# Kernel tuning notes

Measured on AMD Instinct MI355X. Metric: run time of the kernel, lower is better.

Reference implementation:

```python
import jax, jax.numpy as jnp
import numpy as np

B, S, D_MODEL, D_QK, D_VO = 4, 2048, 1024, 128, 128
NEG = -1.0e9


def setup_inputs() -> dict:
    key = jax.random.key(0)
    k1, k2, k3, k4, k5 = jax.random.split(key, 5)
    enc = jax.random.normal(k1, (B, S, D_MODEL), dtype=jnp.float32)
    # causal mask: True means masked (masked_fill), broadcast over batch
    causal = jnp.triu(jnp.ones((S, S), dtype=bool), k=1)
    mask = jnp.broadcast_to(causal, (B, S, S))
    scale = 0.02
    W_q = jax.random.normal(k2, (D_MODEL, D_QK), dtype=jnp.float32) * scale
    W_k = jax.random.normal(k3, (D_MODEL, D_QK), dtype=jnp.float32) * scale
    W_v = jax.random.normal(k4, (D_MODEL, D_VO), dtype=jnp.float32) * scale
    W_o = jax.random.normal(k5, (D_VO, D_MODEL), dtype=jnp.float32) * scale
    return {"encodings": enc, "mask": mask, "W_q": W_q, "W_k": W_k, "W_v": W_v, "W_o": W_o}


def reference(encodings, mask, W_q, W_k, W_v, W_o):
    # q,k: [B,S,d_qk]; v: [B,S,d_vo]
    q = jnp.einsum('bsd,de->bse', encodings, W_q)
    k = jnp.einsum('bsd,de->bse', encodings, W_k)
    v = jnp.einsum('bsd,de->bse', encodings, W_v)
    sims = jnp.einsum('bqe,bke->bqk', q, k) / jnp.asarray(D_QK ** 0.5, q.dtype)
    sims = jnp.where(mask, jnp.asarray(NEG, sims.dtype), sims)
    attn = jax.nn.softmax(sims, axis=-1)  # [B,S,S]
    scores = jnp.einsum('bqk,bke->bqe', attn, v)  # [B,S,d_vo]
    return jnp.einsum('bse,ed->bsd', scores, W_o)  # [B,S,d_model]
```

## Files before the change

kernel.cpp:

```cpp
#include <hip/hip_runtime.h>
#include <hip/hip_bf16.h>
#include <stdint.h>

typedef __attribute__((ext_vector_type(8))) short short8;
typedef __attribute__((ext_vector_type(4))) float floatx4;

using bf16 = __hip_bfloat16;

#define SCALE_L2 0.12751793359133147f

__device__ inline unsigned short f2b(float f) {
    bf16 h = __float2bfloat16(f);
    return *(unsigned short*)&h;
}
__device__ inline float b2f(unsigned short u) {
    union { unsigned int i; float f; } v;
    v.i = ((unsigned int)u) << 16;
    return v.f;
}

__global__ __launch_bounds__(256) void prep_w(const float* __restrict__ Wq,
                                              const float* __restrict__ Wk,
                                              const float* __restrict__ Wv,
                                              const float* __restrict__ Wo,
                                              bf16* __restrict__ Wqkvt,
                                              bf16* __restrict__ Wot) {
    int idx4 = (blockIdx.x * 256 + threadIdx.x) * 4;
    int sel = idx4 >> 17;
    int i = idx4 & 131071;
    if (sel < 3) {
        const float* W = (sel == 0) ? Wq : (sel == 1) ? Wk : Wv;
        float4 v = *(const float4*)&W[i];
        int r = i >> 7, c = i & 127;
        Wqkvt[(size_t)(sel * 128 + c + 0) * 1024 + r] = __float2bfloat16(v.x);
        Wqkvt[(size_t)(sel * 128 + c + 1) * 1024 + r] = __float2bfloat16(v.y);
        Wqkvt[(size_t)(sel * 128 + c + 2) * 1024 + r] = __float2bfloat16(v.z);
        Wqkvt[(size_t)(sel * 128 + c + 3) * 1024 + r] = __float2bfloat16(v.w);
    } else {
        float4 v = *(const float4*)&Wo[i];
        int r = i >> 10, c = i & 1023;
        Wot[(size_t)(c + 0) * 128 + r] = __float2bfloat16(v.x);
        Wot[(size_t)(c + 1) * 128 + r] = __float2bfloat16(v.y);
        Wot[(size_t)(c + 2) * 128 + r] = __float2bfloat16(v.z);
        Wot[(size_t)(c + 3) * 128 + r] = __float2bfloat16(v.w);
    }
}

__global__ __launch_bounds__(256) void gemm_qkv(const float* __restrict__ enc,
                                                const bf16* __restrict__ Bt,
                                                bf16* __restrict__ Qb,
                                                bf16* __restrict__ Kb,
                                                bf16* __restrict__ Vtb) {
    __shared__ bf16 As[64 * 40];
    __shared__ bf16 Bs[64 * 40];

    const int tid = threadIdx.x;
    const int m0 = blockIdx.x * 64;
    const int brow0 = blockIdx.y * 64;
    const int proj = brow0 >> 7;
    const int colb = brow0 & 127;
    const int w = tid >> 6, lane = tid & 63;
    const int wm = (w >> 1) * 32, wn = (w & 1) * 32;
    const int quad = lane >> 4, l16 = lane & 15;

    const int ra = tid >> 2, kq = (tid & 3) * 8;

    floatx4 acc[2][2];
#pragma unroll
    for (int i = 0; i < 2; i++)
#pragma unroll
        for (int j = 0; j < 2; j++) acc[i][j] = (floatx4){0.f, 0.f, 0.f, 0.f};

    float4 pa0 = *(const float4*)&enc[(size_t)(m0 + ra) * 1024 + kq];
    float4 pa1 = *(const float4*)&enc[(size_t)(m0 + ra) * 1024 + kq + 4];
    int4 pb = *(const int4*)&Bt[(size_t)(brow0 + ra) * 1024 + kq];

    for (int k0 = 0; k0 < 1024; k0 += 32) {
        __syncthreads();
        short8 av;
        av[0] = (short)f2b(pa0.x); av[1] = (short)f2b(pa0.y);
        av[2] = (short)f2b(pa0.z); av[3] = (short)f2b(pa0.w);
        av[4] = (short)f2b(pa1.x); av[5] = (short)f2b(pa1.y);
        av[6] = (short)f2b(pa1.z); av[7] = (short)f2b(pa1.w);
        *(short8*)&As[ra * 40 + kq] = av;
        *(int4*)&Bs[ra * 40 + kq] = pb;
        __syncthreads();

        if (k0 + 32 < 1024) {
            pa0 = *(const float4*)&enc[(size_t)(m0 + ra) * 1024 + k0 + 32 + kq];
            pa1 = *(const float4*)&enc[(size_t)(m0 + ra) * 1024 + k0 + 36 + kq];
            pb = *(const int4*)&Bt[(size_t)(brow0 + ra) * 1024 + k0 + 32 + kq];
        }

        short8 a[2], b[2];
#pragma unroll
        for (int mt = 0; mt < 2; mt++)
            a[mt] = *(const short8*)&As[(wm + mt * 16 + l16) * 40 + quad * 8];
#pragma unroll
        for (int nt = 0; nt < 2; nt++)
            b[nt] = *(const short8*)&Bs[(wn + nt * 16 + l16) * 40 + quad * 8];
#pragma unroll
        for (int mt = 0; mt < 2; mt++)
#pragma unroll
            for (int nt = 0; nt < 2; nt++)
                acc[mt][nt] = __builtin_amdgcn_mfma_f32_16x16x32_bf16(a[mt], b[nt], acc[mt][nt], 0, 0, 0);
    }

#pragma unroll
    for (int mt = 0; mt < 2; mt++)
#pragma unroll
        for (int nt = 0; nt < 2; nt++)
#pragma unroll
            for (int r = 0; r < 4; r++) {
                int row = m0 + wm + mt * 16 + quad * 4 + r;
                int col = colb + wn + nt * 16 + l16;
                bf16 h = __float2bfloat16(acc[mt][nt][r]);
                if (proj == 0) {
                    Qb[(size_t)row * 128 + col] = h;
                } else if (proj == 1) {
                    Kb[(size_t)row * 128 + col] = h;
                } else {
                    int bb = row >> 11, ss = row & 2047;
                    Vtb[(size_t)bb * 262144 + (size_t)col * 2048 + ss] = h;
                }
            }
}

__global__ __launch_bounds__(256) void flash_split(const bf16* __restrict__ Q,
                                                   const bf16* __restrict__ K,
                                                   const bf16* __restrict__ Vt,
                                                   bf16* __restrict__ Opb,
                                                   float2* __restrict__ Ml) {
    __shared__ bf16 Ks[64 * 136];
    __shared__ bf16 Vs[128 * 72];
    __shared__ bf16 Ps[4 * 16 * 72];

    const int tid = threadIdx.x;
    const int x = blockIdx.x;
    const int b = x / 272;
    const int id = x - b * 272;
    int m = (int)((__builtin_sqrtf(4.0f * (float)id + 1.0f) - 1.0f) * 0.5f);
    while ((m + 1) * (m + 2) <= id) m++;
    while (m * (m + 1) > id) m--;
    const int rem = id - m * (m + 1);
    const int qt = (rem < m + 1) ? 2 * m : 2 * m + 1;
    const int c = (rem < m + 1) ? rem : rem - (m + 1);
    const int q0 = qt * 64;
    const int start = 2 * c;
    const int end = min(start + 2, qt + 1);

    const int w = tid >> 6, lane = tid & 63;
    const int quad = lane >> 4, l16 = lane & 15;

    const int qrow = q0 + w * 16 + l16;
    const bf16* Qrow = &Q[((size_t)b * 2048 + qrow) * 128];
    short8 qf[4];
#pragma unroll
    for (int k4 = 0; k4 < 4; k4++)
        qf[k4] = *(const short8*)&Qrow[k4 * 32 + quad * 8];

    float m_run = -1.0e30f, l_run = 0.f;
    floatx4 o[8];
#pragma unroll
    for (int d = 0; d < 8; d++) o[d] = (floatx4){0.f, 0.f, 0.f, 0.f};

    int4 kreg[4], vreg[4];
    const int sr[4]  = {(tid + 0) >> 4, (tid + 256) >> 4, (tid + 512) >> 4, (tid + 768) >> 4};
    const int scg    = (tid & 15) * 8;
    const int sr2[4] = {(tid + 0) >> 3, (tid + 256) >> 3, (tid + 512) >> 3, (tid + 768) >> 3};
    const int scg2   = (tid & 7) * 8;

#pragma unroll
    for (int i = 0; i < 4; i++) {
        kreg[i] = *(const int4*)&K[((size_t)b * 2048 + start * 64 + sr[i]) * 128 + scg];
        vreg[i] = *(const int4*)&Vt[(size_t)b * 262144 + (size_t)sr2[i] * 2048 + start * 64 + scg2];
    }

    for (int kt = start; kt < end; kt++) {
        __syncthreads();
#pragma unroll
        for (int i = 0; i < 4; i++) {
            *(int4*)&Ks[sr[i] * 136 + scg] = kreg[i];
            *(int4*)&Vs[sr2[i] * 72 + scg2] = vreg[i];
        }
        __syncthreads();

        if (kt + 1 < end) {
#pragma unroll
            for (int i = 0; i < 4; i++) {
                kreg[i] = *(const int4*)&K[((size_t)b * 2048 + (kt + 1) * 64 + sr[i]) * 128 + scg];
                vreg[i] = *(const int4*)&Vt[(size_t)b * 262144 + (size_t)sr2[i] * 2048 + (kt + 1) * 64 + scg2];
            }
        }

        floatx4 s_acc[4];
#pragma unroll
        for (int nt = 0; nt < 4; nt++) {
            s_acc[nt] = (floatx4){0.f, 0.f, 0.f, 0.f};
#pragma unroll
            for (int k4 = 0; k4 < 4; k4++) {
                short8 kf = *(const short8*)&Ks[(nt * 16 + l16) * 136 + k4 * 32 + quad * 8];
                s_acc[nt] = __builtin_amdgcn_mfma_f32_16x16x32_bf16(kf, qf[k4], s_acc[nt], 0, 0, 0);
            }
        }

        float sv[4][4];
#pragma unroll
        for (int nt = 0; nt < 4; nt++)
#pragma unroll
            for (int r = 0; r < 4; r++) {
                float s = s_acc[nt][r] * SCALE_L2;
                if (kt == qt) {
                    int kcol = kt * 64 + nt * 16 + quad * 4 + r;
                    if (kcol > qrow) s = -1.0e9f;
                }
                sv[nt][r] = s;
            }

        float t0 = fmaxf(fmaxf(sv[0][0], sv[0][1]), fmaxf(sv[0][2], sv[0][3]));
        float t1 = fmaxf(fmaxf(sv[1][0], sv[1][1]), fmaxf(sv[1][2], sv[1][3]));
        float t2 = fmaxf(fmaxf(sv[2][0], sv[2][1]), fmaxf(sv[2][2], sv[2][3]));
        float t3 = fmaxf(fmaxf(sv[3][0], sv[3][1]), fmaxf(sv[3][2], sv[3][3]));
        float tmax = fmaxf(fmaxf(t0, t1), fmaxf(t2, t3));
        tmax = fmaxf(tmax, __shfl_xor(tmax, 16));
        tmax = fmaxf(tmax, __shfl_xor(tmax, 32));

        float mnew = fmaxf(m_run, tmax);
        float alpha = exp2f(m_run - mnew);
        m_run = mnew;

        float rsum = 0.f;
#pragma unroll
        for (int nt = 0; nt < 4; nt++)
#pragma unroll
            for (int r = 0; r < 4; r++) {
                float p = exp2f(sv[nt][r] - mnew);
                sv[nt][r] = p;
                rsum += p;
            }
        rsum += __shfl_xor(rsum, 16);
        rsum += __shfl_xor(rsum, 32);
        l_run = l_run * alpha + rsum;

#pragma unroll
        for (int nt = 0; nt < 4; nt++) {
            ushort4 pk;
            pk.x = f2b(sv[nt][0]); pk.y = f2b(sv[nt][1]);
            pk.z = f2b(sv[nt][2]); pk.w = f2b(sv[nt][3]);
            *(ushort4*)&Ps[w * 1152 + l16 * 72 + nt * 16 + quad * 4] = pk;
        }

#pragma unroll
        for (int d = 0; d < 8; d++) {
            o[d][0] *= alpha; o[d][1] *= alpha; o[d][2] *= alpha; o[d][3] *= alpha;
        }

        short8 pf[2];
#pragma unroll
        for (int k2 = 0; k2 < 2; k2++)
            pf[k2] = *(const short8*)&Ps[w * 1152 + l16 * 72 + k2 * 32 + quad * 8];
#pragma unroll
        for (int d = 0; d < 8; d++)
#pragma unroll
            for (int k2 = 0; k2 < 2; k2++) {
                short8 vf = *(const short8*)&Vs[(d * 16 + l16) * 72 + k2 * 32 + quad * 8];
                o[d] = __builtin_amdgcn_mfma_f32_16x16x32_bf16(vf, pf[k2], o[d], 0, 0, 0);
            }
    }

    const int lrow = w * 16 + l16;
    const size_t obase = ((size_t)x * 64 + lrow) * 128;
#pragma unroll
    for (int d = 0; d < 8; d++) {
        ushort4 pk;
        pk.x = f2b(o[d][0]); pk.y = f2b(o[d][1]);
        pk.z = f2b(o[d][2]); pk.w = f2b(o[d][3]);
        *(ushort4*)&Opb[obase + d * 16 + quad * 4] = pk;
    }
    if (lane < 16) Ml[(size_t)x * 64 + lrow] = make_float2(m_run, l_run);
}

__global__ __launch_bounds__(256) void gemm_out_merge(const bf16* __restrict__ Opb,
                                                      const float2* __restrict__ Ml,
                                                      const bf16* __restrict__ Bt,
                                                      float* __restrict__ C) {
    __shared__ bf16 As[64 * 40];
    __shared__ bf16 Bs[128 * 40];

    const int tid = threadIdx.x;
    const int m0 = blockIdx.x * 64;
    const int n0 = blockIdx.y * 128;
    const int w = tid >> 6, lane = tid & 63;
    const int wm = (w >> 1) * 32, wn = (w & 1) * 64;
    const int quad = lane >> 4, l16 = lane & 15;

    const int ra = tid >> 2, kq = (tid & 3) * 8;
    const int rb0 = tid >> 2, rb1 = (tid + 256) >> 2;

    const int row = m0 + ra;
    const int bb = row >> 11, s = row & 2047;
    const int qt = s >> 6, rl = s & 63;
    const int mm = qt >> 1;
    const int nc = mm + 1;
    const int id0 = bb * 272 + mm * (mm + 1) + ((qt & 1) ? (mm + 1) : 0);

    float M = -1.0e30f;
    for (int j = 0; j < nc; j++)
        M = fmaxf(M, Ml[(size_t)(id0 + j) * 64 + rl].x);
    float wgt[16];
    float L = 0.f;
    for (int j = 0; j < nc; j++) {
        float2 t = Ml[(size_t)(id0 + j) * 64 + rl];
        float wj = exp2f(t.x - M);
        wgt[j] = wj;
        L += t.y * wj;
    }
    float inv = 1.0f / L;
    for (int j = 0; j < nc; j++) wgt[j] *= inv;

    floatx4 acc[2][4];
#pragma unroll
    for (int i = 0; i < 2; i++)
#pragma unroll
        for (int j = 0; j < 4; j++) acc[i][j] = (floatx4){0.f, 0.f, 0.f, 0.f};

    int4 pb0 = *(const int4*)&Bt[(size_t)(n0 + rb0) * 128 + kq];
    int4 pb1 = *(const int4*)&Bt[(size_t)(n0 + rb1) * 128 + kq];

    for (int k0 = 0; k0 < 128; k0 += 32) {
        float a8[8] = {0.f, 0.f, 0.f, 0.f, 0.f, 0.f, 0.f, 0.f};
        const int dq = k0 + kq;
        for (int j = 0; j < nc; j++) {
            const ushort4* p = (const ushort4*)&Opb[((size_t)(id0 + j) * 64 + rl) * 128 + dq];
            ushort4 p0 = p[0], p1 = p[1];
            float wj = wgt[j];
            a8[0] += wj * b2f(p0.x); a8[1] += wj * b2f(p0.y);
            a8[2] += wj * b2f(p0.z); a8[3] += wj * b2f(p0.w);
            a8[4] += wj * b2f(p1.x); a8[5] += wj * b2f(p1.y);
            a8[6] += wj * b2f(p1.z); a8[7] += wj * b2f(p1.w);
        }
        short8 av;
#pragma unroll
        for (int e = 0; e < 8; e++) av[e] = (short)f2b(a8[e]);

        __syncthreads();
        *(short8*)&As[ra * 40 + kq] = av;
        *(int4*)&Bs[rb0 * 40 + kq] = pb0;
        *(int4*)&Bs[rb1 * 40 + kq] = pb1;
        __syncthreads();

        if (k0 + 32 < 128) {
            pb0 = *(const int4*)&Bt[(size_t)(n0 + rb0) * 128 + k0 + 32 + kq];
            pb1 = *(const int4*)&Bt[(size_t)(n0 + rb1) * 128 + k0 + 32 + kq];
        }

        short8 a[2], b[4];
#pragma unroll
        for (int mt = 0; mt < 2; mt++)
            a[mt] = *(const short8*)&As[(wm + mt * 16 + l16) * 40 + quad * 8];
#pragma unroll
        for (int nt = 0; nt < 4; nt++)
            b[nt] = *(const short8*)&Bs[(wn + nt * 16 + l16) * 40 + quad * 8];
#pragma unroll
        for (int mt = 0; mt < 2; mt++)
#pragma unroll
            for (int nt = 0; nt < 4; nt++)
                acc[mt][nt] = __builtin_amdgcn_mfma_f32_16x16x32_bf16(a[mt], b[nt], acc[mt][nt], 0, 0, 0);
    }

#pragma unroll
    for (int mt = 0; mt < 2; mt++)
#pragma unroll
        for (int nt = 0; nt < 4; nt++)
#pragma unroll
            for (int r = 0; r < 4; r++) {
                int orow = m0 + wm + mt * 16 + quad * 4 + r;
                int ocol = n0 + wn + nt * 16 + l16;
                C[(size_t)orow * 1024 + ocol] = acc[mt][nt][r];
            }
}

extern "C" void kernel_launch(void* const* d_in, const int* in_sizes, int n_in,
                              void* d_out, int out_size, void* d_ws, size_t ws_size,
                              hipStream_t stream) {
    const float* enc = (const float*)d_in[0];
    const float* Wq = (const float*)d_in[2];
    const float* Wk = (const float*)d_in[3];
    const float* Wv = (const float*)d_in[4];
    const float* Wo = (const float*)d_in[5];
    float* out = (float*)d_out;

    const size_t MB = 1024 * 1024;
    char* ws = (char*)d_ws;
    bf16*   Opb   = (bf16*)(ws);
    bf16*   Qb    = (bf16*)(ws + 18 * MB);
    bf16*   Kb    = (bf16*)(ws + 20 * MB);
    bf16*   Vtb   = (bf16*)(ws + 22 * MB);
    bf16*   Wqkvt = (bf16*)(ws + 24 * MB);
    bf16*   Wot   = (bf16*)(ws + 24 * MB + 768 * 1024);
    float2* Ml    = (float2*)(ws + 25 * MB);

    dim3 blk(256);
    prep_w<<<512, blk, 0, stream>>>(Wq, Wk, Wv, Wo, Wqkvt, Wot);

    gemm_qkv<<<dim3(128, 6), blk, 0, stream>>>(enc, Wqkvt, Qb, Kb, Vtb);

    flash_split<<<1088, blk, 0, stream>>>(Qb, Kb, Vtb, Opb, Ml);

    gemm_out_merge<<<dim3(128, 8), blk, 0, stream>>>(Opb, Ml, Wot, out);
}
```

Baseline: 219.4 us.

## Fuse all stages into one persistent kernel with grid-wide atomic barriers

Replaces the four separate launches (weight prep, QKV GEMM, split flash attention, merge+output GEMM) with a single persistent kernel of 512 blocks that loops over tiles and uses atomic-counter grid barriers between stages. The flash split changes from chunks of two key tiles to chunks of three, and the merge now appears to be a separate stage writing a bf16 scores buffer before a plain output GEMM. The aim is to remove launch gaps and tail effects between kernels. In exchange it adds spin-wait barrier overhead and a memset, it relies on all 512 blocks being co-resident, and it gives less parallelism per stage.

```diff
diff --git a/kernel.cpp b/kernel.cpp
--- a/kernel.cpp
+++ b/kernel.cpp
@@ -8,6 +8,8 @@
 using bf16 = __hip_bfloat16;
 
 #define SCALE_L2 0.12751793359133147f
+
+#define GRID 512
 
 __device__ inline unsigned short f2b(float f) {
     bf16 h = __float2bfloat16(f);
@@ -19,365 +21,383 @@
     return v.f;
 }
 
-__global__ __launch_bounds__(256) void prep_w(const float* __restrict__ Wq,
-                                              const float* __restrict__ Wk,
-                                              const float* __restrict__ Wv,
-                                              const float* __restrict__ Wo,
-                                              bf16* __restrict__ Wqkvt,
-                                              bf16* __restrict__ Wot) {
-    int idx4 = (blockIdx.x * 256 + threadIdx.x) * 4;
-    int sel = idx4 >> 17;
-    int i = idx4 & 131071;
-    if (sel < 3) {
-        const float* W = (sel == 0) ? Wq : (sel == 1) ? Wk : Wv;
-        float4 v = *(const float4*)&W[i];
-        int r = i >> 7, c = i & 127;
-        Wqkvt[(size_t)(sel * 128 + c + 0) * 1024 + r] = __float2bfloat16(v.x);
-        Wqkvt[(size_t)(sel * 128 + c + 1) * 1024 + r] = __float2bfloat16(v.y);
-        Wqkvt[(size_t)(sel * 128 + c + 2) * 1024 + r] = __float2bfloat16(v.z);
-        Wqkvt[(size_t)(sel * 128 + c + 3) * 1024 + r] = __float2bfloat16(v.w);
-    } else {
-        float4 v = *(const float4*)&Wo[i];
-        int r = i >> 10, c = i & 1023;
-        Wot[(size_t)(c + 0) * 128 + r] = __float2bfloat16(v.x);
-        Wot[(size_t)(c + 1) * 128 + r] = __float2bfloat16(v.y);
-        Wot[(size_t)(c + 2) * 128 + r] = __float2bfloat16(v.z);
-        Wot[(size_t)(c + 3) * 128 + r] = __float2bfloat16(v.w);
-    }
-}
-
-__global__ __launch_bounds__(256) void gemm_qkv(const float* __restrict__ enc,
-                                                const bf16* __restrict__ Bt,
-                                                bf16* __restrict__ Qb,
-                                                bf16* __restrict__ Kb,
-                                                bf16* __restrict__ Vtb) {
-    __shared__ bf16 As[64 * 40];
-    __shared__ bf16 Bs[64 * 40];
-
+__device__ inline int cum3(int qt) {
+    int a = qt / 3, r = qt - 3 * a;
+    return 3 * a * (a + 1) / 2 + r * (a + 1);
+}
+
+__device__ __forceinline__ void gbar(unsigned* bar, unsigned target) {
+    __threadfence();
+    __syncthreads();
+    if (threadIdx.x == 0) {
+        __hip_atomic_fetch_add(bar, 1u, __ATOMIC_RELEASE, __HIP_MEMORY_SCOPE_AGENT);
+        while (__hip_atomic_load(bar, __ATOMIC_ACQUIRE, __HIP_MEMORY_SCOPE_AGENT) < target)
+            __builtin_amdgcn_s_sleep(2);
+    }
+    __syncthreads();
+    __threadfence();
+}
+
+__global__ __launch_bounds__(256, 3) void mega(const float* __restrict__ enc,
+                                               const float* __restrict__ Wq,
+                                               const float* __restrict__ Wk,
+                                               const float* __restrict__ Wv,
+                                               const float* __restrict__ Wo,
+                                               bf16* __restrict__ Wqkvt,
+                                               bf16* __restrict__ Wot,
+                                               bf16* __restrict__ Qb,
+                                               bf16* __restrict__ Kb,
+                                               bf16* __restrict__ Vtb,
+                                               bf16* __restrict__ Opb,
+                                               float2* __restrict__ Ml,
+                                               bf16* __restrict__ Scb,
+                                               float* __restrict__ out,
+                                               unsigned* __restrict__ bar) {
+    __shared__ __align__(16) bf16 smem[22528];
+
+    const int bid = blockIdx.x;
     const int tid = threadIdx.x;
-    const int m0 = blockIdx.x * 64;
-    const int brow0 = blockIdx.y * 64;
-    const int proj = brow0 >> 7;
-    const int colb = brow0 & 127;
-    const int w = tid >> 6, lane = tid & 63;
-    const int wm = (w >> 1) * 32, wn = (w & 1) * 32;
-    const int quad = lane >> 4, l16 = lane & 15;
-
-    const int ra = tid >> 2, kq = (tid & 3) * 8;
-
-    floatx4 acc[2][2];
-#pragma unroll
-    for (int i = 0; i < 2; i++)
-#pragma unroll
-        for (int j = 0; j < 2; j++) acc[i][j] = (floatx4){0.f, 0.f, 0.f, 0.f};
-
-    float4 pa0 = *(const float4*)&enc[(size_t)(m0 + ra) * 1024 + kq];
-    float4 pa1 = *(const float4*)&enc[(size_t)(m0 + ra) * 1024 + kq + 4];
-    int4 pb = *(const int4*)&Bt[(size_t)(brow0 + ra) * 1024 + kq];
-
-    for (int k0 = 0; k0 < 1024; k0 += 32) {
-        __syncthreads();
-        short8 av;
-        av[0] = (short)f2b(pa0.x); av[1] = (short)f2b(pa0.y);
-        av[2] = (short)f2b(pa0.z); av[3] = (short)f2b(pa0.w);
-        av[4] = (short)f2b(pa1.x); av[5] = (short)f2b(pa1.y);
-        av[6] = (short)f2b(pa1.z); av[7] = (short)f2b(pa1.w);
-        *(short8*)&As[ra * 40 + kq] = av;
-        *(int4*)&Bs[ra * 40 + kq] = pb;
-        __syncthreads();
-
-        if (k0 + 32 < 1024) {
-            pa0 = *(const float4*)&enc[(size_t)(m0 + ra) * 1024 + k0 + 32 + kq];
-            pa1 = *(const float4*)&enc[(size_t)(m0 + ra) * 1024 + k0 + 36 + kq];
-            pb = *(const int4*)&Bt[(size_t)(brow0 + ra) * 1024 + k0 + 32 + kq];
-        }
-
-        short8 a[2], b[2];
-#pragma unroll
-        for (int mt = 0; mt < 2; mt++)
-            a[mt] = *(const short8*)&As[(wm + mt * 16 + l16) * 40 + quad * 8];
-#pragma unroll
-        for (int nt = 0; nt < 2; nt++)
-            b[nt] = *(const short8*)&Bs[(wn + nt * 16 + l16) * 40 + quad * 8];
-#pragma unroll
-        for (int mt = 0; mt < 2; mt++)
-#pragma unroll
-            for (int nt = 0; nt < 2; nt++)
-                acc[mt][nt] = __builtin_amdgcn_mfma_f32_16x16x32_bf16(a[mt], b[nt], acc[mt][nt], 0, 0, 0);
-    }
-
-#pragma unroll
-    for (int mt = 0; mt < 2; mt++)
-#pragma unroll
-        for (int nt = 0; nt < 2; nt++)
-#pragma unroll
-            for (int r = 0; r < 4; r++) {
-                int row = m0 + wm + mt * 16 + quad * 4 + r;
-                int col = colb + wn + nt * 16 + l16;
-                bf16 h = __float2bfloat16(acc[mt][nt][r]);
-                if (proj == 0) {
-                    Qb[(size_t)row * 128 + col] = h;
-                } else if (proj == 1) {
-                    Kb[(size_t)row * 128 + col] = h;
-                } else {
-                    int bb = row >> 11, ss = row & 2047;
-                    Vtb[(size_t)bb * 262144 + (size_t)col * 2048 + ss] = h;
-                }
-            }
-}
-
-__global__ __launch_bounds__(256) void flash_split(const bf16* __restrict__ Q,
-                                                   const bf16* __restrict__ K,
-                                                   const bf16* __restrict__ Vt,
-                                                   bf16* __restrict__ Opb,
-                                                   float2* __restrict__ Ml) {
-    __shared__ bf16 Ks[64 * 136];
-    __shared__ bf16 Vs[128 * 72];
-    __shared__ bf16 Ps[4 * 16 * 72];
-
-    const int tid = threadIdx.x;
-    const int x = blockIdx.x;
-    const int b = x / 272;
-    const int id = x - b * 272;
-    int m = (int)((__builtin_sqrtf(4.0f * (float)id + 1.0f) - 1.0f) * 0.5f);
-    while ((m + 1) * (m + 2) <= id) m++;
-    while (m * (m + 1) > id) m--;
-    const int rem = id - m * (m + 1);
-    const int qt = (rem < m + 1) ? 2 * m : 2 * m + 1;
-    const int c = (rem < m + 1) ? rem : rem - (m + 1);
-    const int q0 = qt * 64;
-    const int start = 2 * c;
-    const int end = min(start + 2, qt + 1);
-
     const int w = tid >> 6, lane = tid & 63;
     const int quad = lane >> 4, l16 = lane & 15;
 
-    const int qrow = q0 + w * 16 + l16;
-    const bf16* Qrow = &Q[((size_t)b * 2048 + qrow) * 128];
-    short8 qf[4];
-#pragma unroll
-    for (int k4 = 0; k4 < 4; k4++)
-        qf[k4] = *(const short8*)&Qrow[k4 * 32 + quad * 8];
-
-    float m_run = -1.0e30f, l_run = 0.f;
-    floatx4 o[8];
-#pragma unroll
-    for (int d = 0; d < 8; d++) o[d] = (floatx4){0.f, 0.f, 0.f, 0.f};
-
-    int4 kreg[4], vreg[4];
-    const int sr[4]  = {(tid + 0) >> 4, (tid + 256) >> 4, (tid + 512) >> 4, (tid + 768) >> 4};
-    const int scg    = (tid & 15) * 8;
-    const int sr2[4] = {(tid + 0) >> 3, (tid + 256) >> 3, (tid + 512) >> 3, (tid + 768) >> 3};
-    const int scg2   = (tid & 7) * 8;
-
-#pragma unroll
-    for (int i = 0; i < 4; i++) {
-        kreg[i] = *(const int4*)&K[((size_t)b * 2048 + start * 64 + sr[i]) * 128 + scg];
-        vreg[i] = *(const int4*)&Vt[(size_t)b * 262144 + (size_t)sr2[i] * 2048 + start * 64 + scg2];
-    }
-
-    for (int kt = start; kt < end; kt++) {
-        __syncthreads();
-#pragma unroll
-        for (int i = 0; i < 4; i++) {
-            *(int4*)&Ks[sr[i] * 136 + scg] = kreg[i];
-            *(int4*)&Vs[sr2[i] * 72 + scg2] = vreg[i];
+    {
+        int idx4 = (bid * 256 + tid) * 4;
+        int sel = idx4 >> 17;
+        int i = idx4 & 131071;
+        if (sel < 3) {
+            const float* W = (sel == 0) ? Wq : (sel == 1) ? Wk : Wv;
+            float4 v = *(const float4*)&W[i];
+            int r = i >> 7, c = i & 127;
+            Wqkvt[(size_t)(sel * 128 + c + 0) * 1024 + r] = __float2bfloat16(v.x);
+            Wqkvt[(size_t)(sel * 128 + c + 1) * 1024 + r] = __float2bfloat16(v.y);
+            Wqkvt[(size_t)(sel * 128 + c + 2) * 1024 + r] = __float2bfloat16(v.z);
+            Wqkvt[(size_t)(sel * 128 + c + 3) * 1024 + r] = __float2bfloat16(v.w);
+        } else {
+            float4 v = *(const float4*)&Wo[i];
+            int r = i >> 10, c = i & 1023;
+            Wot[(size_t)(c + 0) * 128 + r] = __float2bfloat16(v.x);
+            Wot[(size_t)(c + 1) * 128 + r] = __float2bfloat16(v.y);
+            Wot[(size_t)(c + 2) * 128 + r] = __float2bfloat16(v.z);
+            Wot[(size_t)(c + 3) * 128 + r] = __float2bfloat16(v.w);
         }
-        __syncthreads();
-
-        if (kt + 1 < end) {
+    }
+    gbar(bar, 1 * GRID);
+
+    {
+        bf16* As = smem;
+        bf16* Bs = smem + 2560;
+        const int wm = (w >> 1) * 32, wn = (w & 1) * 32;
+        const int ra = tid >> 2, kq = (tid & 3) * 8;
+
+        for (int t = bid; t < 768; t += GRID) {
+            const int m0 = (t & 127) * 64;
+            const int brow0 = (t >> 7) * 64;
+            const int proj = brow0 >> 7;
+            const int colb = brow0 & 127;
+
+            floatx4 acc[2][2];
+#pragma unroll
+            for (int i = 0; i < 2; i++)
+#pragma unroll
+                for (int j = 0; j < 2; j++) acc[i][j] = (floatx4){0.f, 0.f, 0.f, 0.f};
+
+            float4 pa0 = *(const float4*)&enc[(size_t)(m0 + ra) * 1024 + kq];
+            float4 pa1 = *(const float4*)&enc[(size_t)(m0 + ra) * 1024 + kq + 4];
+            int4 pb = *(const int4*)&Wqkvt[(size_t)(brow0 + ra) * 1024 + kq];
+
+            for (int k0 = 0; k0 < 1024; k0 += 32) {
+                __syncthreads();
+                short8 av;
+                av[0] = (short)f2b(pa0.x); av[1] = (short)f2b(pa0.y);
+                av[2] = (short)f2b(pa0.z); av[3] = (short)f2b(pa0.w);
+                av[4] = (short)f2b(pa1.x); av[5] = (short)f2b(pa1.y);
+                av[6] = (short)f2b(pa1.z); av[7] = (short)f2b(pa1.w);
+                *(short8*)&As[ra * 40 + kq] = av;
+                *(int4*)&Bs[ra * 40 + kq] = pb;
+                __syncthreads();
+
+                if (k0 + 32 < 1024) {
+                    pa0 = *(const float4*)&enc[(size_t)(m0 + ra) * 1024 + k0 + 32 + kq];
+                    pa1 = *(const float4*)&enc[(size_t)(m0 + ra) * 1024 + k0 + 36 + kq];
+                    pb = *(const int4*)&Wqkvt[(size_t)(brow0 + ra) * 1024 + k0 + 32 + kq];
+                }
+
+                short8 a[2], b[2];
+#pragma unroll
+                for (int mt = 0; mt < 2; mt++)
+                    a[mt] = *(const short8*)&As[(wm + mt * 16 + l16) * 40 + quad * 8];
+#pragma unroll
+                for (int nt = 0; nt < 2; nt++)
+                    b[nt] = *(const short8*)&Bs[(wn + nt * 16 + l16) * 40 + quad * 8];
+#pragma unroll
+                for (int mt = 0; mt < 2; mt++)
+#pragma unroll
+                    for (int nt = 0; nt < 2; nt++)
+                        acc[mt][nt] = __builtin_amdgcn_mfma_f32_16x16x32_bf16(a[mt], b[nt], acc[mt][nt], 0, 0, 0);
+            }
+
+#pragma unroll
+            for (int mt = 0; mt < 2; mt++)
+#pragma unroll
+                for (int nt = 0; nt < 2; nt++)
+#pragma unroll
+                    for (int r = 0; r < 4; r++) {
+                        int row = m0 + wm + mt * 16 + quad * 4 + r;
+                        int col = colb + wn + nt * 16 + l16;
+                        bf16 h = __float2bfloat16(acc[mt][nt][r]);
+                        if (proj == 0) {
+                            Qb[(size_t)row * 128 + col] = h;
+                        } else if (proj == 1) {
+                            Kb[(size_t)row * 128 + col] = h;
+                        } else {
+                            int bb = row >> 11, ss = row & 2047;
+                            Vtb[(size_t)bb * 262144 + (size_t)col * 2048 + ss] = h;
+                        }
+                    }
+            __syncthreads();
+        }
+    }
+    gbar(bar, 2 * GRID);
+
+    {
+        bf16* Ks = smem;
+        bf16* Vs = smem + 8704;
+        bf16* Ps = smem + 17920;
+        const int sr[4]  = {(tid + 0) >> 4, (tid + 256) >> 4, (tid + 512) >> 4, (tid + 768) >> 4};
+        const int scg    = (tid & 15) * 8;
+        const int sr2[4] = {(tid + 0) >> 3, (tid + 256) >> 3, (tid + 512) >> 3, (tid + 768) >> 3};
+        const int scg2   = (tid & 7) * 8;
+
+        for (int x = bid; x < 748; x += GRID) {
+            const int b = x / 187;
+            const int id = x - b * 187;
+            int qt = (int)__builtin_sqrtf(6.0f * (float)id + 1.0f);
+            if (qt > 31) qt = 31;
+            while (cum3(qt + 1) <= id) qt++;
+            while (cum3(qt) > id) qt--;
+            const int c = id - cum3(qt);
+            const int q0 = qt * 64;
+            const int start = 3 * c;
+            const int end = min(start + 3, qt + 1);
+
+            const int qrow = q0 + w * 16 + l16;
+            const bf16* Qrow = &Qb[((size_t)b * 2048 + qrow) * 128];
+            short8 qf[4];
+#pragma unroll
+            for (int k4 = 0; k4 < 4; k4++)
+                qf[k4] = *(const short8*)&Qrow[k4 * 32 + quad * 8];
+
+            float m_run = -1.0e30f, l_run = 0.f;
+            floatx4 o[8];
+#pragma unroll
+            for (int d = 0; d < 8; d++) o[d] = (floatx4){0.f, 0.f, 0.f, 0.f};
+
+            int4 kreg[4], vreg[4];
 #pragma unroll
             for (int i = 0; i < 4; i++) {
-                kreg[i] = *(const int4*)&K[((size_t)b * 2048 + (kt + 1) * 64 + sr[i]) * 128 + scg];
-                vreg[i] = *(const int4*)&Vt[(size_t)b * 262144 + (size_t)sr2[i] * 2048 + (kt + 1) * 64 + scg2];
-            }
+                kreg[i] = *(const int4*)&Kb[((size_t)b * 2048 + start * 64 + sr[i]) * 128 + scg];
+                vreg[i] = *(const int4*)&Vtb[(size_t)b * 262144 + (size_t)sr2[i] * 2048 + start * 64 + scg2];
+            }
+
+            for (int kt = start; kt < end; kt++) {
+                __syncthreads();
+#pragma unroll
+                for (int i = 0; i < 4; i++) {
+                    *(int4*)&Ks[sr[i] * 136 + scg] = kreg[i];
+                    *(int4*)&Vs[sr2[i] * 72 + scg2] = vreg[i];
+                }
+                __syncthreads();
+
+                if (kt + 1 < end) {
+#pragma unroll
+                    for (int i = 0; i < 4; i++) {
+                        kreg[i] = *(const int4*)&Kb[((size_t)b * 2048 + (kt + 1) * 64 + sr[i]) * 128 + scg];
+                        vreg[i] = *(const int4*)&Vtb[(size_t)b * 262144 + (size_t)sr2[i] * 2048 + (kt + 1) * 64 + scg2];
+                    }
+                }
+
+                floatx4 s_acc[4];
+#pragma unroll
+                for (int nt = 0; nt < 4; nt++) {
+                    s_acc[nt] = (floatx4){0.f, 0.f, 0.f, 0.f};
+#pragma unroll
+                    for (int k4 = 0; k4 < 4; k4++) {
+                        short8 kf = *(const short8*)&Ks[(nt * 16 + l16) * 136 + k4 * 32 + quad * 8];
+                        s_acc[nt] = __builtin_amdgcn_mfma_f32_16x16x32_bf16(kf, qf[k4], s_acc[nt], 0, 0, 0);
+                    }
+                }
+
+                float sv[4][4];
+#pragma unroll
+                for (int nt = 0; nt < 4; nt++)
+#pragma unroll
+                    for (int r = 0; r < 4; r++) {
+                        float s = s_acc[nt][r] * SCALE_L2;
+                        if (kt == qt) {
+                            int kcol = kt * 64 + nt * 16 + quad * 4 + r;
+                            if (kcol > qrow) s = -1.0e9f;
+                        }
+                        sv[nt][r] = s;
+                    }
+
+                float t0 = fmaxf(fmaxf(sv[0][0], sv[0][1]), fmaxf(sv[0][2], sv[0][3]));
+                float t1 = fmaxf(fmaxf(sv[1][0], sv[1][1]), fmaxf(sv[1][2], sv[1][3]));
+                float t2 = fmaxf(fmaxf(sv[2][0], sv[2][1]), fmaxf(sv[2][2], sv[2][3]));
+                float t3 = fmaxf(fmaxf(sv[3][0], sv[3][1]), fmaxf(sv[3][2], sv[3][3]));
+                float tmax = fmaxf(fmaxf(t0, t1), fmaxf(t2, t3));
+                tmax = fmaxf(tmax, __shfl_xor(tmax, 16));
+                tmax = fmaxf(tmax, __shfl_xor(tmax, 32));
+
+                float mnew = fmaxf(m_run, tmax);
+                float alpha = exp2f(m_run - mnew);
+                m_run = mnew;
+
+                float rsum = 0.f;
+#pragma unroll
+                for (int nt = 0; nt < 4; nt++)
+#pragma unroll
+                    for (int r = 0; r < 4; r++) {
+                        float p = exp2f(sv[nt][r] - mnew);
+                        sv[nt][r] = p;
+                        rsum += p;
+                    }
+                rsum += __shfl_xor(rsum, 16);
+                rsum += __shfl_xor(rsum, 32);
+                l_run = l_run * alpha + rsum;
+
+#pragma unroll
+                for (int nt = 0; nt < 4; nt++) {
+                    ushort4 pk;
+                    pk.x = f2b(sv[nt][0]); pk.y = f2b(sv[nt][1]);
+                    pk.z = f2b(sv[nt][2]); pk.w = f2b(sv[nt][3]);
+                    *(ushort4*)&Ps[w * 1152 + l16 * 72 + nt * 16 + quad * 4] = pk;
+                }
+
+#pragma unroll
+                for (int d = 0; d < 8; d++) {
+                    o[d][0] *= alpha; o[d][1] *= alpha; o[d][2] *= alpha; o[d][3] *= alpha;
+                }
+
+                short8 pf[2];
+#pragma unroll
+                for (int k2 = 0; k2 < 2; k2++)
+                    pf[k2] = *(const short8*)&Ps[w * 1152 + l16 * 72 + k2 * 32 + quad * 8];
+#pragma unroll
+                for (int d = 0; d < 8; d++)
+#pragma unroll
+                    for (int k2 = 0; k2 < 2; k2++) {
+                        short8 vf = *(const short8*)&Vs[(d * 16 + l16) * 72 + k2 * 32 + quad * 8];
+                        o[d] = __builtin_amdgcn_mfma_f32_16x16x32_bf16(vf, pf[k2], o[d], 0, 0, 0);
+                    }
+            }
+
+            const int lrow = w * 16 + l16;
+            const size_t obase = ((size_t)x * 64 + lrow) * 128;
+#pragma unroll
+            for (int d = 0; d < 8; d++) {
+                ushort4 pk;
+                pk.x = f2b(o[d][0]); pk.y = f2b(o[d][1]);
+                pk.z = f2b(o[d][2]); pk.w = f2b(o[d][3]);
+                *(ushort4*)&Opb[obase + d * 16 + quad * 4] = pk;
+            }
+            if (lane < 16) Ml[(size_t)x * 64 + lrow] = make_float2(m_run, l_run);
+            __syncthreads();
         }
-
-        floatx4 s_acc[4];
-#pragma unroll
-        for (int nt = 0; nt < 4; nt++) {
-            s_acc[nt] = (floatx4){0.f, 0.f, 0.f, 0.f};
-#pragma unroll
-            for (int k4 = 0; k4 < 4; k4++) {
-                short8 kf = *(const short8*)&Ks[(nt * 16 + l16) * 136 + k4 * 32 + quad * 8];
-                s_acc[nt] = __builtin_amdgcn_mfma_f32_16x16x32_bf16(kf, qf[k4], s_acc[nt], 0, 0, 0);
-            }
+    }
+    gbar(bar, 3 * GRID);
+
+    {
+        const int gtid = bid * 256 + tid;
+        for (int task = gtid; task < 262144; task += GRID * 256) {
+            int row = task >> 5, dg = (task & 31) * 4;
+            int b = row >> 11, s = row & 2047;
+            int qt = s >> 6, rl = s & 63;
+            int nc = (qt + 3) / 3;
+            int id0 = b * 187 + cum3(qt);
+
+            float M = -1.0e30f;
+            for (int j = 0; j < nc; j++)
+                M = fmaxf(M, Ml[(size_t)(id0 + j) * 64 + rl].x);
+            float L = 0.f;
+            float a0 = 0.f, a1 = 0.f, a2 = 0.f, a3 = 0.f;
+            for (int j = 0; j < nc; j++) {
+                float2 t = Ml[(size_t)(id0 + j) * 64 + rl];
+                float wj = exp2f(t.x - M);
+                L += t.y * wj;
+                ushort4 p = *(const ushort4*)&Opb[((size_t)(id0 + j) * 64 + rl) * 128 + dg];
+                a0 += wj * b2f(p.x); a1 += wj * b2f(p.y);
+                a2 += wj * b2f(p.z); a3 += wj * b2f(p.w);
+            }
+            float inv = 1.0f / L;
+            ushort4 o;
+            o.x = f2b(a0 * inv); o.y = f2b(a1 * inv);
+            o.z = f2b(a2 * inv); o.w = f2b(a3 * inv);
+            *(ushort4*)&Scb[(size_t)row * 128 + dg] = o;
         }
-
-        float sv[4][4];
-#pragma unroll
-        for (int nt = 0; nt < 4; nt++)
-#pragma unroll
-            for (int r = 0; r < 4; r++) {
-                float s = s_acc[nt][r] * SCALE_L2;
-                if (kt == qt) {
-                    int kcol = kt * 64 + nt * 16 + quad * 4 + r;
-                    if (kcol > qrow) s = -1.0e9f;
-                }
-                sv[nt][r] = s;
-            }
-
-        float t0 = fmaxf(fmaxf(sv[0][0], sv[0][1]), fmaxf(sv[0][2], sv[0][3]));
-        float t1 = fmaxf(fmaxf(sv[1][0], sv[1][1]), fmaxf(sv[1][2], sv[1][3]));
-        float t2 = fmaxf(fmaxf(sv[2][0], sv[2][1]), fmaxf(sv[2][2], sv[2][3]));
-        float t3 = fmaxf(fmaxf(sv[3][0], sv[3][1]), fmaxf(sv[3][2], sv[3][3]));
-        float tmax = fmaxf(fmaxf(t0, t1), fmaxf(t2, t3));
-        tmax = fmaxf(tmax, __shfl_xor(tmax, 16));
-        tmax = fmaxf(tmax, __shfl_xor(tmax, 32));
-
-        float mnew = fmaxf(m_run, tmax);
-        float alpha = exp2f(m_run - mnew);
-        m_run = mnew;
-
-        float rsum = 0.f;
-#pragma unroll
-        for (int nt = 0; nt < 4; nt++)
-#pragma unroll
-            for (int r = 0; r < 4; r++) {
-                float p = exp2f(sv[nt][r] - mnew);
-                sv[nt][r] = p;
-                rsum += p;
-            }
-        rsum += __shfl_xor(rsum, 16);
-        rsum += __shfl_xor(rsum, 32);
-        l_run = l_run * alpha + rsum;
-
-#pragma unroll
-        for (int nt = 0; nt < 4; nt++) {
-            ushort4 pk;
-            pk.x = f2b(sv[nt][0]); pk.y = f2b(sv[nt][1]);
-            pk.z = f2b(sv[nt][2]); pk.w = f2b(sv[nt][3]);
-            *(ushort4*)&Ps[w * 1152 + l16 * 72 + nt * 16 + quad * 4] = pk;
+    }
+    gbar(bar, 4 * GRID);
+
+    {
+        bf16* As = smem;
+        bf16* Bs = smem + 2560;
+        const int wm = (w >> 1) * 32, wn = (w & 1) * 64;
+        const int ra = tid >> 2, kq = (tid & 3) * 8;
+        const int rb0 = tid >> 2, rb1 = (tid + 256) >> 2;
+
+        for (int t = bid; t < 1024; t += GRID) {
+            const int m0 = (t & 127) * 64;
+            const int n0 = (t >> 7) * 128;
+
+            floatx4 acc[2][4];
+#pragma unroll
+            for (int i = 0; i < 2; i++)
+#pragma unroll
+                for (int j = 0; j < 4; j++) acc[i][j] = (floatx4){0.f, 0.f, 0.f, 0.f};
+
+            int4 pa  = *(const int4*)&Scb[(size_t)(m0 + ra) * 128 + kq];
+            int4 pb0 = *(const int4*)&Wot[(size_t)(n0 + rb0) * 128 + kq];
+            int4 pb1 = *(const int4*)&Wot[(size_t)(n0 + rb1) * 128 + kq];
+
+            for (int k0 = 0; k0 < 128; k0 += 32) {
+                __syncthreads();
+                *(int4*)&As[ra * 40 + kq] = pa;
+                *(int4*)&Bs[rb0 * 40 + kq] = pb0;
+                *(int4*)&Bs[rb1 * 40 + kq] = pb1;
+                __syncthreads();
+
+                if (k0 + 32 < 128) {
+                    pa  = *(const int4*)&Scb[(size_t)(m0 + ra) * 128 + k0 + 32 + kq];
+                    pb0 = *(const int4*)&Wot[(size_t)(n0 + rb0) * 128 + k0 + 32 + kq];
+                    pb1 = *(const int4*)&Wot[(size_t)(n0 + rb1) * 128 + k0 + 32 + kq];
+                }
+
+                short8 a[2], b[4];
+#pragma unroll
+                for (int mt = 0; mt < 2; mt++)
+                    a[mt] = *(const short8*)&As[(wm + mt * 16 + l16) * 40 + quad * 8];
+#pragma unroll
+                for (int nt = 0; nt < 4; nt++)
+                    b[nt] = *(const short8*)&Bs[(wn + nt * 16 + l16) * 40 + quad * 8];
+#pragma unroll
+                for (int mt = 0; mt < 2; mt++)
+#pragma unroll
+                    for (int nt = 0; nt < 4; nt++)
+                        acc[mt][nt] = __builtin_amdgcn_mfma_f32_16x16x32_bf16(a[mt], b[nt], acc[mt][nt], 0, 0, 0);
+            }
+
+#pragma unroll
+            for (int mt = 0; mt < 2; mt++)
+#pragma unroll
+                for (int nt = 0; nt < 4; nt++)
+#pragma unroll
+                    for (int r = 0; r < 4; r++) {
+                        int orow = m0 + wm + mt * 16 + quad * 4 + r;
+                        int ocol = n0 + wn + nt * 16 + l16;
+                        out[(size_t)orow * 1024 + ocol] = acc[mt][nt][r];
+                    }
+            __syncthreads();
         }
-
-#pragma unroll
-        for (int d = 0; d < 8; d++) {
-            o[d][0] *= alpha; o[d][1] *= alpha; o[d][2] *= alpha; o[d][3] *= alpha;
-        }
-
-        short8 pf[2];
-#pragma unroll
-        for (int k2 = 0; k2 < 2; k2++)
-            pf[k2] = *(const short8*)&Ps[w * 1152 + l16 * 72 + k2 * 32 + quad * 8];
-#pragma unroll
-        for (int d = 0; d < 8; d++)
-#pragma unroll
-            for (int k2 = 0; k2 < 2; k2++) {
-                short8 vf = *(const short8*)&Vs[(d * 16 + l16) * 72 + k2 * 32 + quad * 8];
-                o[d] = __builtin_amdgcn_mfma_f32_16x16x32_bf16(vf, pf[k2], o[d], 0, 0, 0);
-            }
-    }
-
-    const int lrow = w * 16 + l16;
-    const size_t obase = ((size_t)x * 64 + lrow) * 128;
-#pragma unroll
-    for (int d = 0; d < 8; d++) {
-        ushort4 pk;
-        pk.x = f2b(o[d][0]); pk.y = f2b(o[d][1]);
-        pk.z = f2b(o[d][2]); pk.w = f2b(o[d][3]);
-        *(ushort4*)&Opb[obase + d * 16 + quad * 4] = pk;
-    }
-    if (lane < 16) Ml[(size_t)x * 64 + lrow] = make_float2(m_run, l_run);
-}
-
-__global__ __launch_bounds__(256) void gemm_out_merge(const bf16* __restrict__ Opb,
-                                                      const float2* __restrict__ Ml,
-                                                      const bf16* __restrict__ Bt,
-                                                      float* __restrict__ C) {
-    __shared__ bf16 As[64 * 40];
-    __shared__ bf16 Bs[128 * 40];
-
-    const int tid = threadIdx.x;
-    const int m0 = blockIdx.x * 64;
-    const int n0 = blockIdx.y * 128;
-    const int w = tid >> 6, lane = tid & 63;
-    const int wm = (w >> 1) * 32, wn = (w & 1) * 64;
-    const int quad = lane >> 4, l16 = lane & 15;
-
-    const int ra = tid >> 2, kq = (tid & 3) * 8;
-    const int rb0 = tid >> 2, rb1 = (tid + 256) >> 2;
-
-    const int row = m0 + ra;
-    const int bb = row >> 11, s = row & 2047;
-    const int qt = s >> 6, rl = s & 63;
-    const int mm = qt >> 1;
-    const int nc = mm + 1;
-    const int id0 = bb * 272 + mm * (mm + 1) + ((qt & 1) ? (mm + 1) : 0);
-
-    float M = -1.0e30f;
-    for (int j = 0; j < nc; j++)
-        M = fmaxf(M, Ml[(size_t)(id0 + j) * 64 + rl].x);
-    float wgt[16];
-    float L = 0.f;
-    for (int j = 0; j < nc; j++) {
-        float2 t = Ml[(size_t)(id0 + j) * 64 + rl];
-        float wj = exp2f(t.x - M);
-        wgt[j] = wj;
-        L += t.y * wj;
-    }
-    float inv = 1.0f / L;
-    for (int j = 0; j < nc; j++) wgt[j] *= inv;
-
-    floatx4 acc[2][4];
-#pragma unroll
-    for (int i = 0; i < 2; i++)
-#pragma unroll
-        for (int j = 0; j < 4; j++) acc[i][j] = (floatx4){0.f, 0.f, 0.f, 0.f};
-
-    int4 pb0 = *(const int4*)&Bt[(size_t)(n0 + rb0) * 128 + kq];
-    int4 pb1 = *(const int4*)&Bt[(size_t)(n0 + rb1) * 128 + kq];
-
-    for (int k0 = 0; k0 < 128; k0 += 32) {
-        float a8[8] = {0.f, 0.f, 0.f, 0.f, 0.f, 0.f, 0.f, 0.f};
-        const int dq = k0 + kq;
-        for (int j = 0; j < nc; j++) {
-            const ushort4* p = (const ushort4*)&Opb[((size_t)(id0 + j) * 64 + rl) * 128 + dq];
-            ushort4 p0 = p[0], p1 = p[1];
-            float wj = wgt[j];
-            a8[0] += wj * b2f(p0.x); a8[1] += wj * b2f(p0.y);
-            a8[2] += wj * b2f(p0.z); a8[3] += wj * b2f(p0.w);
-            a8[4] += wj * b2f(p1.x); a8[5] += wj * b2f(p1.y);
-            a8[6] += wj * b2f(p1.z); a8[7] += wj * b2f(p1.w);
-        }
-        short8 av;
-#pragma unroll
-        for (int e = 0; e < 8; e++) av[e] = (short)f2b(a8[e]);
-
-        __syncthreads();
-        *(short8*)&As[ra * 40 + kq] = av;
-        *(int4*)&Bs[rb0 * 40 + kq] = pb0;
-        *(int4*)&Bs[rb1 * 40 + kq] = pb1;
-        __syncthreads();
-
-        if (k0 + 32 < 128) {
-            pb0 = *(const int4*)&Bt[(size_t)(n0 + rb0) * 128 + k0 + 32 + kq];
-            pb1 = *(const int4*)&Bt[(size_t)(n0 + rb1) * 128 + k0 + 32 + kq];
-        }
-
-        short8 a[2], b[4];
-#pragma unroll
-        for (int mt = 0; mt < 2; mt++)
-            a[mt] = *(const short8*)&As[(wm + mt * 16 + l16) * 40 + quad * 8];
-#pragma unroll
-        for (int nt = 0; nt < 4; nt++)
-            b[nt] = *(const short8*)&Bs[(wn + nt * 16 + l16) * 40 + quad * 8];
-#pragma unroll
-        for (int mt = 0; mt < 2; mt++)
-#pragma unroll
-            for (int nt = 0; nt < 4; nt++)
-                acc[mt][nt] = __builtin_amdgcn_mfma_f32_16x16x32_bf16(a[mt], b[nt], acc[mt][nt], 0, 0, 0);
-    }
-
-#pragma unroll
-    for (int mt = 0; mt < 2; mt++)
-#pragma unroll
-        for (int nt = 0; nt < 4; nt++)
-#pragma unroll
-            for (int r = 0; r < 4; r++) {
-                int orow = m0 + wm + mt * 16 + quad * 4 + r;
-                int ocol = n0 + wn + nt * 16 + l16;
-                C[(size_t)orow * 1024 + ocol] = acc[mt][nt][r];
-            }
+    }
 }
 
 extern "C" void kernel_launch(void* const* d_in, const int* in_sizes, int n_in,
@@ -392,20 +412,18 @@
 
     const size_t MB = 1024 * 1024;
     char* ws = (char*)d_ws;
-    bf16*   Opb   = (bf16*)(ws);
-    bf16*   Qb    = (bf16*)(ws + 18 * MB);
-    bf16*   Kb    = (bf16*)(ws + 20 * MB);
-    bf16*   Vtb   = (bf16*)(ws + 22 * MB);
-    bf16*   Wqkvt = (bf16*)(ws + 24 * MB);
-    bf16*   Wot   = (bf16*)(ws + 24 * MB + 768 * 1024);
-    float2* Ml    = (float2*)(ws + 25 * MB);
-
-    dim3 blk(256);
-    prep_w<<<512, blk, 0, stream>>>(Wq, Wk, Wv, Wo, Wqkvt, Wot);
-
-    gemm_qkv<<<dim3(128, 6), blk, 0, stream>>>(enc, Wqkvt, Qb, Kb, Vtb);
-
-    flash_split<<<1088, blk, 0, stream>>>(Qb, Kb, Vtb, Opb, Ml);
-
-    gemm_out_merge<<<dim3(128, 8), blk, 0, stream>>>(Opb, Ml, Wot, out);
-}
+    bf16*     Opb   = (bf16*)(ws);
+    bf16*     Qb    = (bf16*)(ws + 13 * MB);
+    bf16*     Kb    = (bf16*)(ws + 15 * MB);
+    bf16*     Vtb   = (bf16*)(ws + 17 * MB);
+    bf16*     Scb   = (bf16*)(ws + 19 * MB);
+    bf16*     Wqkvt = (bf16*)(ws + 21 * MB);
+    bf16*     Wot   = (bf16*)(ws + 21 * MB + 768 * 1024);
+    float2*   Ml    = (float2*)(ws + 22 * MB);
+    unsigned* bar   = (unsigned*)(ws + 23 * MB);
+
+    hipMemsetAsync(bar, 0, 64, stream);
+
+    mega<<<GRID, 256, 0, stream>>>(enc, Wq, Wk, Wv, Wo, Wqkvt, Wot,
+                                   Qb, Kb, Vtb, Opb, Ml, Scb, out, bar);
+}
```

New measurement: 875.3 us. 299% more time.
